# Kernel tuning notes

Measured on AMD Instinct MI355X. Metric: run time of the kernel, lower is better.

## Reference

```python
import jax, jax.numpy as jnp
import numpy as np

N = 8000   # nodes
E = 32000  # edges
B = 64     # graphs in batch
V = 5000   # vocab
D = 200    # embed dim; 20 tokens/node * 200 = 4000 = conv1 in_dim
T = 20


def setup_inputs() -> dict:
    key = jax.random.key(0)
    ks = jax.random.split(key, 12)
    return {
        "x": jax.random.randint(ks[0], (N, T), 0, V),
        "edge_index": jax.random.randint(ks[1], (2, E), 0, N),
        "batch": jnp.sort(jax.random.randint(ks[2], (N,), 0, B)),
        "emb": jax.random.normal(ks[3], (V, D), jnp.float32) * 0.02,
        "W1": jax.random.normal(ks[4], (4000, 6000), jnp.float32) * 0.01,
        "b1": jnp.zeros((6000,), jnp.float32),
        "W2": jax.random.normal(ks[5], (6000, 6000), jnp.float32) * 0.01,
        "b2": jnp.zeros((6000,), jnp.float32),
        "Wl1": jax.random.normal(ks[6], (6000, 3000), jnp.float32) * 0.01,
        "bl1": jnp.zeros((3000,), jnp.float32),
        "Wl2": jax.random.normal(ks[7], (3000, 4), jnp.float32) * 0.01,
        "bl2": jnp.zeros((4,), jnp.float32),
    }


def gcn_conv(h, W, b, src, dst, n):
    """PyG GCNConv: x' = D^-1/2 (A+I) D^-1/2 (x W) + b; src/dst include self-loops."""
    h = h @ W  # [n, out]
    deg = jax.ops.segment_sum(jnp.ones(dst.shape[0], h.dtype), dst, num_segments=n)
    dinv = jnp.where(deg > 0, jax.lax.rsqrt(deg), 0.0)
    norm = dinv[src] * dinv[dst]  # [E+n]
    agg = jax.ops.segment_sum(h[src] * norm[:, None], dst, num_segments=n)
    return agg + b


def reference(x, edge_index, batch, emb, W1, b1, W2, b2, Wl1, bl1, Wl2, bl2):
    n = x.shape[0]
    h = emb[x].reshape(n, -1)  # [N, 4000]
    loops = jnp.arange(n)
    src = jnp.concatenate([edge_index[0], loops])
    dst = jnp.concatenate([edge_index[1], loops])
    h = jax.nn.leaky_relu(gcn_conv(h, W1, b1, src, dst, n))  # dropout: identity in eval
    h = jax.nn.leaky_relu(gcn_conv(h, W2, b2, src, dst, n))
    g = jax.ops.segment_max(h, batch, num_segments=B)  # global_max_pool -> [B, 6000]
    g = jax.nn.leaky_relu(g @ Wl1 + bl1)
    return jax.nn.leaky_relu(g @ Wl2 + bl2)  # [B, 4]
```

## Files before the change

### kernel.cpp

```cpp
#include <hip/hip_runtime.h>
#include <hip/hip_bf16.h>

#define Nn 8000
#define Ee 32000
#define Bb 64
#define Dembed 200
#define Ttok 20
#define Mp 8192
#define K1 4096
#define K2 6144
#define L1p 3072
#define LCHUNK 256
#define NCH 24

#define GBM 256
#define GBN 256
#define GBK 64
#define ABUF (GBM * GBK)
#define BUFE (2 * ABUF)

#define LRELU(v) ((v) > 0.f ? (v) : 0.01f * (v))

typedef __attribute__((ext_vector_type(4))) float f32x4;
typedef __attribute__((ext_vector_type(8))) short s16x8;
typedef __attribute__((ext_vector_type(4))) short s16x4;

#define GLL16(gp, lp) __builtin_amdgcn_global_load_lds( \
    (const __attribute__((address_space(1))) void*)(gp), \
    (__attribute__((address_space(3))) void*)(lp), 16, 0, 0)

__device__ __forceinline__ float b2f(short s) {
    union { unsigned u; float f; } c;
    c.u = ((unsigned)(unsigned short)s) << 16;
    return c.f;
}
__device__ __forceinline__ short f2b(float f) {
    __hip_bfloat16 h = __float2bfloat16(f);
    return __builtin_bit_cast(short, h);
}

__global__ __launch_bounds__(256)
void k_gather(const int* __restrict__ x, const float* __restrict__ emb,
              short* __restrict__ h0, int Wp)
{
    const int i = blockIdx.x;
    __shared__ int tok[Ttok];
    if (threadIdx.x < Ttok) tok[threadIdx.x] = x[i * Ttok + threadIdx.x];
    __syncthreads();
    for (int c = threadIdx.x; c < Wp; c += 256) {
        float v = 0.f;
        if (c < Ttok * Dembed) {
            int t = c / Dembed;
            int d = c - t * Dembed;
            v = emb[(long)tok[t] * Dembed + d];
        }
        h0[(long)i * Wp + c] = f2b(v);
    }
}

__global__ void k_deg(const int* __restrict__ dst, int* __restrict__ indeg) {
    int e = blockIdx.x * 256 + threadIdx.x;
    if (e < Ee) atomicAdd(&indeg[dst[e]], 1);
}

__global__ __launch_bounds__(1024)
void k_scan(const int* __restrict__ indeg, int* __restrict__ rowptr,
            float* __restrict__ dinv, int n)
{
    __shared__ int sums[1024];
    const int t = threadIdx.x;
    const int base = t * 8;
    int loc[8];
    int s = 0;
#pragma unroll
    for (int j = 0; j < 8; ++j) {
        int v = (base + j < n) ? indeg[base + j] : 0;
        loc[j] = s; s += v;
    }
    sums[t] = s;
    __syncthreads();
    for (int off = 1; off < 1024; off <<= 1) {
        int v = sums[t];
        int add = (t >= off) ? sums[t - off] : 0;
        __syncthreads();
        sums[t] = v + add;
        __syncthreads();
    }
    const int prev = (t == 0) ? 0 : sums[t - 1];
#pragma unroll
    for (int j = 0; j < 8; ++j)
        if (base + j < n) {
            rowptr[base + j] = prev + loc[j];
            dinv[base + j] = rsqrtf((float)indeg[base + j] + 1.0f);
        }
    if (t == 1023) rowptr[n] = sums[1023];
}

__global__ void k_fill(const int* __restrict__ src, const int* __restrict__ dst,
                       const int* __restrict__ rowptr, int* __restrict__ fillc,
                       int* __restrict__ csr) {
    int e = blockIdx.x * 256 + threadIdx.x;
    if (e < Ee) {
        int d = dst[e];
        int pos = rowptr[d] + atomicAdd(&fillc[d], 1);
        csr[pos] = src[e];
    }
}

template<int NG>
__global__ __launch_bounds__(256)
void k_agg(const short* __restrict__ Hin, short* __restrict__ Hout,
           const float* __restrict__ dinv, const int* __restrict__ rowptr,
           const int* __restrict__ csr, int Wp)
{
    const int i = blockIdx.x;
    const int tid = threadIdx.x;
    const float di = dinv[i];
    const float wself = di * di;
    const long rowi = (long)i * Wp;
    float acc[NG * 8];
#pragma unroll
    for (int gI = 0; gI < NG; ++gI) {
        s16x8 v = *(const s16x8*)(Hin + rowi + gI * 2048 + tid * 8);
#pragma unroll
        for (int j = 0; j < 8; ++j) acc[gI * 8 + j] = wself * b2f(v[j]);
    }
    const int e0 = rowptr[i], e1 = rowptr[i + 1];
    for (int e = e0; e < e1; ++e) {
        const int s = csr[e];
        const float w = dinv[s] * di;
        const long rows = (long)s * Wp;
#pragma unroll
        for (int gI = 0; gI < NG; ++gI) {
            s16x8 v = *(const s16x8*)(Hin + rows + gI * 2048 + tid * 8);
#pragma unroll
            for (int j = 0; j < 8; ++j) acc[gI * 8 + j] += w * b2f(v[j]);
        }
    }
#pragma unroll
    for (int gI = 0; gI < NG; ++gI) {
        s16x8 o;
#pragma unroll
        for (int j = 0; j < 8; ++j) o[j] = f2b(acc[gI * 8 + j]);
        *(s16x8*)(Hout + rowi + gI * 2048 + tid * 8) = o;
    }
}

__global__ __launch_bounds__(256)
void k_transpose(const float* __restrict__ In, short* __restrict__ Out,
                 int K, int N, int Kp, int Np)
{
    __shared__ float tile[32][33];
    const int k0 = blockIdx.x * 32;
    const int n0 = blockIdx.y * 32;
    const int tid = threadIdx.x;
    const int ln = tid & 31, lk = tid >> 5;
#pragma unroll
    for (int kk = lk; kk < 32; kk += 8) {
        int k = k0 + kk, n = n0 + ln;
        tile[kk][ln] = (k < K && n < N) ? In[(long)k * N + n] : 0.f;
    }
    __syncthreads();
    const int kq = tid & 7, nn = tid >> 3;
    s16x4 o;
#pragma unroll
    for (int j = 0; j < 4; ++j) o[j] = f2b(tile[kq * 4 + j][nn]);
    *(s16x4*)(&Out[(long)(n0 + nn) * Kp + k0 + kq * 4]) = o;
}

__global__ __launch_bounds__(512, 2)
void k_gemm8p(const short* __restrict__ A, const short* __restrict__ Bt,
              short* __restrict__ C, const float* __restrict__ bias,
              int K, int Np, int Nreal, int nbx)
{
    __shared__ short lds[2 * BUFE];

    const int tid  = threadIdx.x;
    const int lane = tid & 63;
    const int wid  = tid >> 6;
    const int wm   = wid >> 2;
    const int wn   = wid & 3;

    const int cpx = (int)gridDim.x >> 3;
    const int bid = (int)blockIdx.x;
    const int swz = (bid & 7) * cpx + (bid >> 3);
    const int bx = swz % nbx;
    const int by = swz / nbx;

    const int rq = tid >> 3;
    const int kq = ((tid & 7) << 3) ^ ((rq & 7) << 3);
    const short* Abase = A  + ((long)by * GBM + rq) * K + kq;
    const short* Bbase = Bt + ((long)bx * GBN + rq) * K + kq;

#define ST2(bb, t2, base, ldoff, c0_, c1_) do { \
    const short* g0_ = (base) + (long)((c0_) * 64) * K + (long)(t2) * GBK; \
    const short* g1_ = (base) + (long)((c1_) * 64) * K + (long)(t2) * GBK; \
    GLL16(g0_, lds + (bb) * BUFE + (ldoff) + (c0_) * 4096 + tid * 8); \
    GLL16(g1_, lds + (bb) * BUFE + (ldoff) + (c1_) * 4096 + tid * 8); \
  } while (0)

    const int fr  = lane & 15;
    const int kb8 = (lane >> 4) << 3;
    const int xm  = (fr & 7) << 3;
    const int ck0 = kb8 ^ xm;
    const int ck1 = (32 + kb8) ^ xm;
    const int aoff = (wm * 128 + fr) * 64;
    const int boff = ABUF + (wn * 64 + fr) * 64;

    f32x4 acc[8][4] = {};
    s16x8 av_a[4], av_b[4], bv1[4], bv3[4];

    const int NT = K >> 6;

    ST2(0, 0, Bbase, ABUF, 0, 1);
    ST2(0, 0, Bbase, ABUF, 2, 3);
    ST2(0, 0, Abase, 0,    0, 2);
    ST2(0, 0, Abase, 0,    1, 3);
    asm volatile("s_waitcnt vmcnt(0)" ::: "memory");
    __builtin_amdgcn_s_barrier();

    int buf = 0;
    for (int t = 0; t < NT; ++t) {
        const short* lb = lds + buf * BUFE;
        const int nb = buf ^ 1;
        const bool pf = (t + 1 < NT);

#pragma unroll
        for (int n = 0; n < 4; ++n) bv1[n] = *(const s16x8*)(lb + boff + n * 1024 + ck0);
#pragma unroll
        for (int m = 0; m < 4; ++m) av_a[m] = *(const s16x8*)(lb + aoff + m * 1024 + ck0);
        if (pf) ST2(nb, t + 1, Bbase, ABUF, 0, 1);
#pragma unroll
        for (int m = 0; m < 4; ++m) av_b[m] = *(const s16x8*)(lb + aoff + (4 + m) * 1024 + ck0);
        __builtin_amdgcn_s_setprio(1);
#pragma unroll
        for (int m = 0; m < 4; ++m)
#pragma unroll
            for (int n = 0; n < 4; ++n)
                acc[m][n] = __builtin_amdgcn_mfma_f32_16x16x32_bf16(av_a[m], bv1[n], acc[m][n], 0, 0, 0);
        __builtin_amdgcn_s_setprio(0);
        if (pf) ST2(nb, t + 1, Bbase, ABUF, 2, 3);
#pragma unroll
        for (int n = 0; n < 4; ++n) bv3[n] = *(const s16x8*)(lb + boff + n * 1024 + ck1);
#pragma unroll
        for (int m = 0; m < 4; ++m) av_a[m] = *(const s16x8*)(lb + aoff + (4 + m) * 1024 + ck1);
        __builtin_amdgcn_s_setprio(1);
#pragma unroll
        for (int m = 0; m < 4; ++m)
#pragma unroll
            for (int n = 0; n < 4; ++n)
                acc[4 + m][n] = __builtin_amdgcn_mfma_f32_16x16x32_bf16(av_b[m], bv1[n], acc[4 + m][n], 0, 0, 0);
        __builtin_amdgcn_s_setprio(0);
        if (pf) ST2(nb, t + 1, Abase, 0, 0, 2);
#pragma unroll
        for (int m = 0; m < 4; ++m) av_b[m] = *(const s16x8*)(lb + aoff + m * 1024 + ck1);
        __builtin_amdgcn_s_setprio(1);
#pragma unroll
        for (int m = 0; m < 4; ++m)
#pragma unroll
            for (int n = 0; n < 4; ++n)
                acc[4 + m][n] = __builtin_amdgcn_mfma_f32_16x16x32_bf16(av_a[m], bv3[n], acc[4 + m][n], 0, 0, 0);
        __builtin_amdgcn_s_setprio(0);
        if (pf) ST2(nb, t + 1, Abase, 0, 1, 3);
        __builtin_amdgcn_s_setprio(1);
#pragma unroll
        for (int m = 0; m < 4; ++m)
#pragma unroll
            for (int n = 0; n < 4; ++n)
                acc[m][n] = __builtin_amdgcn_mfma_f32_16x16x32_bf16(av_b[m], bv3[n], acc[m][n], 0, 0, 0);
        __builtin_amdgcn_s_setprio(0);

        asm volatile("s_waitcnt vmcnt(0)" ::: "memory");
        __builtin_amdgcn_s_barrier();
        buf = nb;
    }

    const int rr = (lane >> 4) << 2;
#pragma unroll
    for (int n = 0; n < 4; ++n) {
        const long col = (long)bx * GBN + wn * 64 + n * 16 + fr;
        const float bvv = (col < Nreal) ? bias[col] : 0.f;
#pragma unroll
        for (int m = 0; m < 8; ++m) {
#pragma unroll
            for (int j = 0; j < 4; ++j) {
                const long row = (long)by * GBM + wm * 128 + m * 16 + rr + j;
                float v = acc[m][n][j] + bvv;
                v = LRELU(v);
                C[row * Np + col] = f2b(v);
            }
        }
    }
#undef ST2
}

__global__ void k_bptr(const int* __restrict__ batch, int* __restrict__ bptr) {
    int i = blockIdx.x * 256 + threadIdx.x;
    if (i >= Nn) return;
    int b = batch[i];
    int pb = (i == 0) ? -1 : batch[i - 1];
    for (int bb = pb + 1; bb <= b; ++bb) bptr[bb] = i;
    if (i == Nn - 1)
        for (int bb = b + 1; bb <= Bb; ++bb) bptr[bb] = Nn;
}

__global__ __launch_bounds__(256)
void k_pool(const short* __restrict__ h2, const int* __restrict__ bptr,
            float* __restrict__ g, int Wp) {
    const int c8 = blockIdx.x * 256 + threadIdx.x;
    const int b = blockIdx.y;
    const short* base = h2 + (long)c8 * 8;
    float mx[8];
#pragma unroll
    for (int j = 0; j < 8; ++j) mx[j] = -INFINITY;
    const int i0 = bptr[b], i1 = bptr[b + 1];
    for (int i = i0; i < i1; ++i) {
        s16x8 v = *(const s16x8*)(base + (long)i * Wp);
#pragma unroll
        for (int j = 0; j < 8; ++j) mx[j] = fmaxf(mx[j], b2f(v[j]));
    }
#pragma unroll
    for (int j = 0; j < 8; ++j) g[(long)b * Wp + c8 * 8 + j] = mx[j];
}

__global__ __launch_bounds__(256)
void k_lin1_part(const float* __restrict__ g, const float* __restrict__ Wl1,
                 float* __restrict__ part) {
    __shared__ float gs[64][65];
    __shared__ float Ws[64][64];
    const int tid = threadIdx.x;
    const int jc = blockIdx.x * 64;
    const int k0 = blockIdx.y * LCHUNK;
    const int k1 = min(6000, k0 + LCHUNK);
    const int r = tid & 63;
    const int jb = (tid >> 6) * 16;
    float acc[16] = {};
    for (int kc = k0; kc < k1; kc += 64) {
#pragma unroll
        for (int p = 0; p < 16; ++p) {
            int el = p * 256 + tid;
            int rr = el >> 6, kk = el & 63;
            gs[rr][kk] = (kc + kk < k1) ? g[rr * K2 + kc + kk] : 0.f;
            Ws[rr][kk] = (kc + rr < k1 && jc + kk < 3000)
                         ? Wl1[(long)(kc + rr) * 3000 + jc + kk] : 0.f;
        }
        __syncthreads();
#pragma unroll
        for (int k = 0; k < 64; ++k) {
            float a = gs[r][k];
#pragma unroll
            for (int jj = 0; jj < 16; ++jj)
                acc[jj] += a * Ws[k][jb + jj];
        }
        __syncthreads();
    }
    float* prow = part + ((long)blockIdx.y * 64 + r) * L1p + jc + jb;
#pragma unroll
    for (int jj = 0; jj < 16; ++jj) prow[jj] = acc[jj];
}

__global__ __launch_bounds__(256)
void k_lin1_red(const float* __restrict__ part, const float* __restrict__ bl1,
                float* __restrict__ g1) {
    int idx = blockIdx.x * 256 + threadIdx.x;
    if (idx >= 64 * 3000) return;
    int r = idx / 3000;
    int c = idx - r * 3000;
    float s = bl1[c];
#pragma unroll
    for (int p = 0; p < NCH; ++p)
        s += part[((long)p * 64 + r) * L1p + c];
    g1[r * L1p + c] = LRELU(s);
}

__global__ __launch_bounds__(256)
void k_lin2(const float* __restrict__ g1, const float* __restrict__ Wl2,
            const float* __restrict__ bl2, float* __restrict__ out) {
    const int r = blockIdx.x;
    const int tid = threadIdx.x;
    float a0 = 0, a1 = 0, a2 = 0, a3 = 0;
    for (int k = tid; k < 3000; k += 256) {
        float gv = g1[r * L1p + k];
        const float* w = Wl2 + (long)k * 4;
        a0 += gv * w[0]; a1 += gv * w[1]; a2 += gv * w[2]; a3 += gv * w[3];
    }
    __shared__ float red[256][4];
    red[tid][0] = a0; red[tid][1] = a1; red[tid][2] = a2; red[tid][3] = a3;
    __syncthreads();
    for (int s = 128; s > 0; s >>= 1) {
        if (tid < s) {
            red[tid][0] += red[tid + s][0]; red[tid][1] += red[tid + s][1];
            red[tid][2] += red[tid + s][2]; red[tid][3] += red[tid + s][3];
        }
        __syncthreads();
    }
    if (tid < 4) {
        float v = red[0][tid] + bl2[tid];
        out[r * 4 + tid] = LRELU(v);
    }
}

extern "C" void kernel_launch(void* const* d_in, const int* in_sizes, int n_in,
                              void* d_out, int out_size, void* d_ws, size_t ws_size,
                              hipStream_t stream)
{
    const int*   x     = (const int*)d_in[0];
    const int*   ei    = (const int*)d_in[1];
    const int*   batch = (const int*)d_in[2];
    const float* emb   = (const float*)d_in[3];
    const float* W1    = (const float*)d_in[4];
    const float* b1    = (const float*)d_in[5];
    const float* W2    = (const float*)d_in[6];
    const float* b2    = (const float*)d_in[7];
    const float* Wl1   = (const float*)d_in[8];
    const float* bl1   = (const float*)d_in[9];
    const float* Wl2   = (const float*)d_in[10];
    const float* bl2   = (const float*)d_in[11];
    float* out = (float*)d_out;

    const int* esrc = ei;
    const int* edst = ei + Ee;

    const size_t MiB = 1ull << 20;
    char* W = (char*)d_ws;
    short* h0b  = (short*)(W + 0);
    short* Ah0b = (short*)(W + 64 * MiB);
    short* W2t  = (short*)(W + 96 * MiB);
    short* W1t  = (short*)(W + 128 * MiB);
    short* h1b  = (short*)(W + 176 * MiB);
    short* Ah1b = (short*)(W + 0);
    short* h2b  = h1b;
    float* part = (float*)(W + 0);
    char* S = W + 272 * MiB;
    int*   indeg  = (int*)(S);
    float* dinv   = (float*)(S + 32 * 1024);
    int*   rowptr = (int*)(S + 64 * 1024);
    int*   fillc  = (int*)(S + 96 * 1024);
    int*   csr    = (int*)(S + 128 * 1024);
    int*   bptr   = (int*)(S + 256 * 1024);
    float* g      = (float*)(S + 320 * 1024);
    float* g1     = (float*)(S + 320 * 1024 + 2 * MiB);

    hipMemsetAsync(indeg, 0, Nn * sizeof(int), stream);
    hipMemsetAsync(fillc, 0, Nn * sizeof(int), stream);

    k_gather<<<Nn, 256, 0, stream>>>(x, emb, h0b, K1);
    k_deg<<<(Ee + 255) / 256, 256, 0, stream>>>(edst, indeg);
    k_scan<<<1, 1024, 0, stream>>>(indeg, rowptr, dinv, Nn);
    k_fill<<<(Ee + 255) / 256, 256, 0, stream>>>(esrc, edst, rowptr, fillc, csr);

    const int nbx = K2 / GBN;
    const int nwg = nbx * (Mp / GBM);

    k_agg<2><<<Nn, 256, 0, stream>>>(h0b, Ah0b, dinv, rowptr, csr, K1);
    k_transpose<<<dim3(K1 / 32, K2 / 32), 256, 0, stream>>>(W1, W1t, 4000, 6000, K1, K2);
    k_gemm8p<<<nwg, 512, 0, stream>>>(Ah0b, W1t, h1b, b1, K1, K2, 6000, nbx);

    k_transpose<<<dim3(K2 / 32, K2 / 32), 256, 0, stream>>>(W2, W2t, 6000, 6000, K2, K2);
    k_agg<3><<<Nn, 256, 0, stream>>>(h1b, Ah1b, dinv, rowptr, csr, K2);
    k_gemm8p<<<nwg, 512, 0, stream>>>(Ah1b, W2t, h2b, b2, K2, K2, 6000, nbx);

    k_bptr<<<(Nn + 255) / 256, 256, 0, stream>>>(batch, bptr);
    k_pool<<<dim3(K2 / 2048, Bb), 256, 0, stream>>>(h2b, bptr, g, K2);
    k_lin1_part<<<dim3(L1p / 64, NCH), 256, 0, stream>>>(g, Wl1, part);
    k_lin1_red<<<(64 * 3000 + 255) / 256, 256, 0, stream>>>(part, bl1, g1);
    k_lin2<<<Bb, 256, 0, stream>>>(g1, Wl2, bl2, out);
}
```

Measured before the change: 1.402 ms.

## Switch GEMM to 4 waves each computing a 128x128 subtile

The 256x256 GEMM tile is now computed by 4 waves instead of 8, with each wave owning a 128x128 output subtile and 64 accumulators instead of 32. Each thread issues twice as many global-to-LDS loads, and the per-k-step schedule is simplified to two phases. The aim is more MFMA work per LDS fragment read, which lowers LDS traffic per FLOP. The cost is much higher register pressure (256 accumulator VGPRs plus fragments), one workgroup per CU, and fewer waves to hide latency.

```diff
diff --git a/kernel.cpp b/kernel.cpp
--- a/kernel.cpp
+++ b/kernel.cpp
@@ -168,8 +168,8 @@
     *(s16x4*)(&Out[(long)(n0 + nn) * Kp + k0 + kq * 4]) = o;
 }
 
-__global__ __launch_bounds__(512, 2)
-void k_gemm8p(const short* __restrict__ A, const short* __restrict__ Bt,
+__global__ __launch_bounds__(256, 1)
+void k_gemm4w(const short* __restrict__ A, const short* __restrict__ Bt,
               short* __restrict__ C, const float* __restrict__ bias,
               int K, int Np, int Nreal, int nbx)
 {
@@ -178,8 +178,8 @@
     const int tid  = threadIdx.x;
     const int lane = tid & 63;
     const int wid  = tid >> 6;
-    const int wm   = wid >> 2;
-    const int wn   = wid & 3;
+    const int wm   = wid >> 1;
+    const int wn   = wid & 1;
 
     const int cpx = (int)gridDim.x >> 3;
     const int bid = (int)blockIdx.x;
@@ -192,11 +192,11 @@
     const short* Abase = A  + ((long)by * GBM + rq) * K + kq;
     const short* Bbase = Bt + ((long)bx * GBN + rq) * K + kq;
 
-#define ST2(bb, t2, base, ldoff, c0_, c1_) do { \
-    const short* g0_ = (base) + (long)((c0_) * 64) * K + (long)(t2) * GBK; \
-    const short* g1_ = (base) + (long)((c1_) * 64) * K + (long)(t2) * GBK; \
-    GLL16(g0_, lds + (bb) * BUFE + (ldoff) + (c0_) * 4096 + tid * 8); \
-    GLL16(g1_, lds + (bb) * BUFE + (ldoff) + (c1_) * 4096 + tid * 8); \
+#define STC(bb, t2, base, ldoff, c_) do { \
+    const short* g_ = (base) + (long)((c_) * 64) * K + (long)(t2) * GBK; \
+    short* l_ = lds + (bb) * BUFE + (ldoff) + (c_) * 4096 + tid * 8; \
+    GLL16(g_, l_); \
+    GLL16(g_ + 32 * (long)K, l_ + 2048); \
   } while (0)
 
     const int fr  = lane & 15;
@@ -205,17 +205,17 @@
     const int ck0 = kb8 ^ xm;
     const int ck1 = (32 + kb8) ^ xm;
     const int aoff = (wm * 128 + fr) * 64;
-    const int boff = ABUF + (wn * 64 + fr) * 64;
-
-    f32x4 acc[8][4] = {};
-    s16x8 av_a[4], av_b[4], bv1[4], bv3[4];
+    const int boff = ABUF + (wn * 128 + fr) * 64;
+
+    f32x4 acc[8][8] = {};
+    s16x8 av0[8], bv0[8], av1[8], bv1[8];
 
     const int NT = K >> 6;
 
-    ST2(0, 0, Bbase, ABUF, 0, 1);
-    ST2(0, 0, Bbase, ABUF, 2, 3);
-    ST2(0, 0, Abase, 0,    0, 2);
-    ST2(0, 0, Abase, 0,    1, 3);
+#pragma unroll
+    for (int c = 0; c < 4; ++c) STC(0, 0, Abase, 0, c);
+#pragma unroll
+    for (int c = 0; c < 4; ++c) STC(0, 0, Bbase, ABUF, c);
     asm volatile("s_waitcnt vmcnt(0)" ::: "memory");
     __builtin_amdgcn_s_barrier();
 
@@ -226,48 +226,34 @@
         const bool pf = (t + 1 < NT);
 
 #pragma unroll
-        for (int n = 0; n < 4; ++n) bv1[n] = *(const s16x8*)(lb + boff + n * 1024 + ck0);
-#pragma unroll
-        for (int m = 0; m < 4; ++m) av_a[m] = *(const s16x8*)(lb + aoff + m * 1024 + ck0);
-        if (pf) ST2(nb, t + 1, Bbase, ABUF, 0, 1);
-#pragma unroll
-        for (int m = 0; m < 4; ++m) av_b[m] = *(const s16x8*)(lb + aoff + (4 + m) * 1024 + ck0);
+        for (int m = 0; m < 8; ++m) av0[m] = *(const s16x8*)(lb + aoff + m * 1024 + ck0);
+#pragma unroll
+        for (int n = 0; n < 8; ++n) bv0[n] = *(const s16x8*)(lb + boff + n * 1024 + ck0);
+        if (pf) {
+#pragma unroll
+            for (int c = 0; c < 4; ++c) STC(nb, t + 1, Abase, 0, c);
+        }
+#pragma unroll
+        for (int m = 0; m < 8; ++m) av1[m] = *(const s16x8*)(lb + aoff + m * 1024 + ck1);
+#pragma unroll
+        for (int n = 0; n < 8; ++n) bv1[n] = *(const s16x8*)(lb + boff + n * 1024 + ck1);
+        if (pf) {
+#pragma unroll
+            for (int c = 0; c < 4; ++c) STC(nb, t + 1, Bbase, ABUF, c);
+        }
         __builtin_amdgcn_s_setprio(1);
 #pragma unroll
-        for (int m = 0; m < 4; ++m)
-#pragma unroll
-            for (int n = 0; n < 4; ++n)
-                acc[m][n] = __builtin_amdgcn_mfma_f32_16x16x32_bf16(av_a[m], bv1[n], acc[m][n], 0, 0, 0);
+        for (int m = 0; m < 8; ++m)
+#pragma unroll
+            for (int n = 0; n < 8; ++n)
+                acc[m][n] = __builtin_amdgcn_mfma_f32_16x16x32_bf16(av0[m], bv0[n], acc[m][n], 0, 0, 0);
         __builtin_amdgcn_s_setprio(0);
-        if (pf) ST2(nb, t + 1, Bbase, ABUF, 2, 3);
-#pragma unroll
-        for (int n = 0; n < 4; ++n) bv3[n] = *(const s16x8*)(lb + boff + n * 1024 + ck1);
-#pragma unroll
-        for (int m = 0; m < 4; ++m) av_a[m] = *(const s16x8*)(lb + aoff + (4 + m) * 1024 + ck1);
         __builtin_amdgcn_s_setprio(1);
 #pragma unroll
-        for (int m = 0; m < 4; ++m)
-#pragma unroll
-            for (int n = 0; n < 4; ++n)
-                acc[4 + m][n] = __builtin_amdgcn_mfma_f32_16x16x32_bf16(av_b[m], bv1[n], acc[4 + m][n], 0, 0, 0);
-        __builtin_amdgcn_s_setprio(0);
-        if (pf) ST2(nb, t + 1, Abase, 0, 0, 2);
-#pragma unroll
-        for (int m = 0; m < 4; ++m) av_b[m] = *(const s16x8*)(lb + aoff + m * 1024 + ck1);
-        __builtin_amdgcn_s_setprio(1);
-#pragma unroll
-        for (int m = 0; m < 4; ++m)
-#pragma unroll
-            for (int n = 0; n < 4; ++n)
-                acc[4 + m][n] = __builtin_amdgcn_mfma_f32_16x16x32_bf16(av_a[m], bv3[n], acc[4 + m][n], 0, 0, 0);
-        __builtin_amdgcn_s_setprio(0);
-        if (pf) ST2(nb, t + 1, Abase, 0, 1, 3);
-        __builtin_amdgcn_s_setprio(1);
-#pragma unroll
-        for (int m = 0; m < 4; ++m)
-#pragma unroll
-            for (int n = 0; n < 4; ++n)
-                acc[m][n] = __builtin_amdgcn_mfma_f32_16x16x32_bf16(av_b[m], bv3[n], acc[m][n], 0, 0, 0);
+        for (int m = 0; m < 8; ++m)
+#pragma unroll
+            for (int n = 0; n < 8; ++n)
+                acc[m][n] = __builtin_amdgcn_mfma_f32_16x16x32_bf16(av1[m], bv1[n], acc[m][n], 0, 0, 0);
         __builtin_amdgcn_s_setprio(0);
 
         asm volatile("s_waitcnt vmcnt(0)" ::: "memory");
@@ -277,8 +263,8 @@
 
     const int rr = (lane >> 4) << 2;
 #pragma unroll
-    for (int n = 0; n < 4; ++n) {
-        const long col = (long)bx * GBN + wn * 64 + n * 16 + fr;
+    for (int n = 0; n < 8; ++n) {
+        const long col = (long)bx * GBN + wn * 128 + n * 16 + fr;
         const float bvv = (col < Nreal) ? bias[col] : 0.f;
 #pragma unroll
         for (int m = 0; m < 8; ++m) {
@@ -291,7 +277,7 @@
             }
         }
     }
-#undef ST2
+#undef STC
 }
 
 __global__ void k_bptr(const int* __restrict__ batch, int* __restrict__ bptr) {
@@ -454,11 +440,11 @@
 
     k_agg<2><<<Nn, 256, 0, stream>>>(h0b, Ah0b, dinv, rowptr, csr, K1);
     k_transpose<<<dim3(K1 / 32, K2 / 32), 256, 0, stream>>>(W1, W1t, 4000, 6000, K1, K2);
-    k_gemm8p<<<nwg, 512, 0, stream>>>(Ah0b, W1t, h1b, b1, K1, K2, 6000, nbx);
+    k_gemm4w<<<nwg, 256, 0, stream>>>(Ah0b, W1t, h1b, b1, K1, K2, 6000, nbx);
 
     k_transpose<<<dim3(K2 / 32, K2 / 32), 256, 0, stream>>>(W2, W2t, 6000, 6000, K2, K2);
     k_agg<3><<<Nn, 256, 0, stream>>>(h1b, Ah1b, dinv, rowptr, csr, K2);
-    k_gemm8p<<<nwg, 512, 0, stream>>>(Ah1b, W2t, h2b, b2, K2, K2, 6000, nbx);
+    k_gemm4w<<<nwg, 256, 0, stream>>>(Ah1b, W2t, h2b, b2, K2, K2, 6000, nbx);
 
     k_bptr<<<(Nn + 255) / 256, 256, 0, stream>>>(batch, bptr);
     k_pool<<<dim3(K2 / 2048, Bb), 256, 0, stream>>>(h2b, bptr, g, K2);
```

Measured after the change: 1.407 ms. About the same (+0.4%).
